# Optimization experiments

Hardware: AMD Instinct MI355X
Metric: run time of the kernel (lower is better)

Reference implementation:

```python
import jax, jax.numpy as jnp
import numpy as np

N_ATOMS = 10000
N_PAIRS = 100000
H = 64          # hidden_channels
R = 32          # number_of_radial_basis_functions
MAX_Z = 100
CUTOFF = 0.5    # nm (radial_max_distance), min = 0.0


def cosine_cutoff(d):
    # 0.5*(cos(pi*d/rc)+1) for d < rc else 0
    return jnp.where(d < CUTOFF, 0.5 * (jnp.cos(jnp.pi * d / CUTOFF) + 1.0), 0.0)


def expnormal_rbf(d):
    # ExpNormal smearing (TorchMD/TensorNet style), cutoff_lower = 0
    start = float(np.exp(-CUTOFF))
    means = jnp.linspace(start, 1.0, R, dtype=d.dtype)            # [R]
    beta = (2.0 / R * (1.0 - start)) ** -2
    alpha = 5.0 / CUTOFF
    return jnp.exp(-beta * (jnp.exp(-alpha * d)[:, None] - means) ** 2)  # [P,R]


def vector_to_skewtensor(v):
    x, y, z = v[:, 0], v[:, 1], v[:, 2]
    o = jnp.zeros_like(x)
    return jnp.stack([o, -z, y, z, o, -x, -y, x, o], axis=-1).reshape(-1, 3, 3)


def vector_to_symtensor(v):
    t = v[:, :, None] * v[:, None, :]                              # [P,3,3]
    tr3 = (t[:, 0, 0] + t[:, 1, 1] + t[:, 2, 2]) / 3.0
    return t - tr3[:, None, None] * jnp.eye(3, dtype=v.dtype)


def setup_inputs() -> dict:
    key = jax.random.key(0)
    ks = jax.random.split(key, 20)
    atomic_numbers = jax.random.randint(ks[0], (N_ATOMS,), 0, MAX_Z)
    pair_indices = jax.random.randint(ks[1], (2, N_PAIRS), 0, N_ATOMS)
    r_ij = jax.random.normal(ks[2], (N_PAIRS, 3), dtype=jnp.float32) * 0.12  # ~0.2 nm norms
    d_ij = jnp.linalg.norm(r_ij, axis=-1, keepdims=True) + 1e-6
    s = 0.1
    p = {
        'emb':    jax.random.normal(ks[3], (MAX_Z, H)) * s,
        'emb2_w': jax.random.normal(ks[4], (H, 2 * H)) * s,
        'emb2_b': jnp.zeros((H,)),
        'dp1_w':  jax.random.normal(ks[5], (H, R)) * s,
        'dp1_b':  jnp.zeros((H,)),
        'dp2_w':  jax.random.normal(ks[6], (H, R)) * s,
        'dp2_b':  jnp.zeros((H,)),
        'dp3_w':  jax.random.normal(ks[7], (H, R)) * s,
        'dp3_b':  jnp.zeros((H,)),
        'lt0_w':  jax.random.normal(ks[8], (H, H)) * s,
        'lt1_w':  jax.random.normal(ks[9], (H, H)) * s,
        'lt2_w':  jax.random.normal(ks[10], (H, H)) * s,
        'ls1_w':  jax.random.normal(ks[11], (2 * H, H)) * s,
        'ls1_b':  jnp.zeros((2 * H,)),
        'ls2_w':  jax.random.normal(ks[12], (3 * H, 2 * H)) * s,
        'ls2_b':  jnp.zeros((3 * H,)),
        'ln_g':   jnp.ones((H,)),
        'ln_b':   jnp.zeros((H,)),
    }
    return dict(atomic_numbers=atomic_numbers, pair_indices=pair_indices,
                d_ij=d_ij, r_ij=r_ij, **p)


def reference(atomic_numbers, pair_indices, d_ij, r_ij,
              emb, emb2_w, emb2_b, dp1_w, dp1_b, dp2_w, dp2_b, dp3_w, dp3_b,
              lt0_w, lt1_w, lt2_w, ls1_w, ls1_b, ls2_w, ls2_b, ln_g, ln_b):
    n_atoms = atomic_numbers.shape[0]
    src = pair_indices[0]
    # atomic number message Zij: concat(emb[i], emb[j]) -> Linear
    zi = emb[atomic_numbers]                                      # [N,H]
    zij = jnp.concatenate([zi[src], zi[pair_indices[1]]], axis=-1)  # [P,2H]
    Zij = zij @ emb2_w.T + emb2_b                                 # [P,H]
    d = d_ij[:, 0]                                                # [P]
    unit = r_ij / d_ij                                            # [P,3]
    rc = cosine_cutoff(d)                                         # [P]
    rbf = expnormal_rbf(d) * rc[:, None]                          # [P,R]
    C = rc[:, None] * Zij                                         # [P,H]
    f1 = (rbf @ dp1_w.T + dp1_b) * C                              # [P,H]
    f2 = (rbf @ dp2_w.T + dp2_b) * C * 10.0                       # Angstrom scale
    f3 = (rbf @ dp3_w.T + dp3_b) * C * 100.0
    eye = jnp.eye(3, dtype=r_ij.dtype)
    skew = vector_to_skewtensor(unit)                             # [P,3,3]
    sym = vector_to_symtensor(unit)                               # [P,3,3]
    Iij = f1[:, :, None, None] * eye                              # [P,H,3,3]
    Aij = f2[:, :, None, None] * skew[:, None]
    Sij = f3[:, :, None, None] * sym[:, None]
    I = jax.ops.segment_sum(Iij, src, num_segments=n_atoms)       # [N,H,3,3]
    A = jax.ops.segment_sum(Aij, src, num_segments=n_atoms)
    S = jax.ops.segment_sum(Sij, src, num_segments=n_atoms)
    # tensor_norm -> LayerNorm -> scalar MLP
    tn = jnp.sum((I + A + S) ** 2, axis=(-2, -1))                 # [N,H]
    mu = tn.mean(-1, keepdims=True)
    var = tn.var(-1, keepdims=True)
    norm = (tn - mu) / jnp.sqrt(var + 1e-5) * ln_g + ln_b
    norm = jax.nn.silu(norm @ ls1_w.T + ls1_b)
    norm = jax.nn.silu(norm @ ls2_w.T + ls2_b)                    # [N,3H]
    norm = norm.reshape(-1, H, 3)
    I = jnp.einsum('nhij,gh->ngij', I, lt0_w) * norm[:, :, 0][:, :, None, None]
    A = jnp.einsum('nhij,gh->ngij', A, lt1_w) * norm[:, :, 1][:, :, None, None]
    S = jnp.einsum('nhij,gh->ngij', S, lt2_w) * norm[:, :, 2][:, :, None, None]
    return I + A + S
```

## Files before the change

### kernel.cpp

```cpp
#include <hip/hip_runtime.h>
#include <hip/hip_bf16.h>

#define N_ATOMS 10000
#define N_PAIRS 100000
#define HH 64
#define MAXZ 100

typedef _Float16 h2_t __attribute__((ext_vector_type(2)));

constexpr float RBF_START = 0.6065306597126334f;
constexpr float RBF_STEP  = (1.0f - RBF_START) / 31.0f;
constexpr float RBF_BETA  = 1.0f / ((0.0625f * (1.0f - RBF_START)) * (0.0625f * (1.0f - RBF_START)));
constexpr float LOG2E     = 1.4426950408889634f;
constexpr float NEG_ALPHA_L2 = -10.0f * LOG2E;
constexpr float NEG_BETA_L2  = -RBF_BETA * LOG2E;

#define OFF_EMB   0
#define OFF_W2    6400
#define OFF_B2    14592
#define OFF_D1W   14656
#define OFF_D1B   16704
#define OFF_D2W   16768
#define OFF_D2B   18816
#define OFF_D3W   18880
#define OFF_D3B   20928
#define OFF_LT0   20992
#define OFF_LT1   25088
#define OFF_LT2   29184
#define OFF_L1W   33280
#define OFF_L1B   41472
#define OFF_L2W   41600
#define OFF_L2B   66176
#define OFF_LNG   66368
#define OFF_LNB   66432
#define N_PARAMF  66496

#define PH_DP   0
#define PH_L1   3072
#define PH_L2   7168
#define PH_LT   19456
#define PH_N    25600

#define WS_WF     0
#define WS_CNT    266240
#define WS_OFF    307200
#define WS_CUR    348160
#define WS_T1     389120
#define WS_T2     414720
#define WS_PH     440320
#define WS_DPK    542720
#define WS_ZNL    2142720
#define WS_RBF    2542720
#define WS_ACCH   8942720

__device__ __forceinline__ float bf2f(unsigned short u) {
    return __uint_as_float(((unsigned int)u) << 16);
}
__device__ __forceinline__ float fexp2(float x) { return __builtin_amdgcn_exp2f(x); }
__device__ __forceinline__ float fcos2pi(float x) { return __builtin_amdgcn_cosf(x); }
__device__ __forceinline__ float fsilu(float x) { return x / (1.0f + fexp2(-LOG2E * x)); }
__device__ __forceinline__ h2_t u2h(unsigned u) { return __builtin_bit_cast(h2_t, u); }
__device__ __forceinline__ unsigned packh2(float a, float b) {
    h2_t v; v.x = (_Float16)a; v.y = (_Float16)b;
    return __builtin_bit_cast(unsigned, v);
}

#if __has_builtin(__builtin_amdgcn_fdot2)
__device__ __forceinline__ float FDOT2(h2_t a, h2_t b, float c) {
    return __builtin_amdgcn_fdot2(a, b, c, false);
}
#else
__device__ __forceinline__ float FDOT2(h2_t a, h2_t b, float c) {
    return c + (float)a.x * (float)b.x + (float)a.y * (float)b.y;
}
#endif
__device__ __forceinline__ float dot16v(uint4 a, uint4 b, float acc) {
    acc = FDOT2(u2h(a.x), u2h(b.x), acc);
    acc = FDOT2(u2h(a.y), u2h(b.y), acc);
    acc = FDOT2(u2h(a.z), u2h(b.z), acc);
    acc = FDOT2(u2h(a.w), u2h(b.w), acc);
    return acc;
}
__device__ __forceinline__ float dot16h(const uint4* w, const uint4* x, float acc) {
    return dot16v(*w, *x, acc);
}

__device__ int classify64(const unsigned short* b, int lane) {
    unsigned short x = b[lane];
    int e = (x >> 7) & 0xFF;
    bool implaus = (x != 0) && (e < 96 || e > 133);
    bool zeroeven = ((lane & 1) == 0) && (x == 0);
    unsigned long long mi = __ballot(implaus);
    unsigned long long mz = __ballot(zeroeven);
    if (__popcll(mz) == 32) return 0;
    if (__popcll(mi) >= 8) return 0;
    return 1;
}

struct ConvArgs { const void* src[18]; float* dst; };

__global__ void k_prep(ConvArgs a, const int* __restrict__ pidx, int* __restrict__ cnt) {
    const int sizes[18] = {6400,8192,64,2048,64,2048,64,2048,64,4096,4096,4096,8192,128,24576,192,64,64};
    __shared__ int fl;
    if (threadIdx.x < 64) {
        int f = classify64((const unsigned short*)a.src[0], threadIdx.x);
        if (threadIdx.x == 0) fl = f;
    }
    __syncthreads();
    int t = blockIdx.x * 256 + threadIdx.x;
    if (t < N_PARAMF) {
        int acc = 0, seg = 0, off = t;
        #pragma unroll
        for (int i = 0; i < 18; ++i) {
            if (t >= acc && t < acc + sizes[i]) { seg = i; off = t - acc; }
            acc += sizes[i];
        }
        if (fl == 1) a.dst[t] = bf2f(((const unsigned short*)a.src[seg])[off]);
        else         a.dst[t] = ((const float*)a.src[seg])[off];
    }
    if (t < N_PAIRS) atomicAdd(&cnt[pidx[t]], 1);
}

__global__ void k_scantab(const float* __restrict__ WF, float* __restrict__ T1,
                          float* __restrict__ T2, unsigned* __restrict__ PH,
                          const int* __restrict__ cnt, int* __restrict__ offs,
                          int* __restrict__ cur) {
    __shared__ int buf[1024];
    if (blockIdx.x == 0) {
        int tid = threadIdx.x;
        int base = tid * 10;
        int c[10]; int s = 0;
        #pragma unroll
        for (int i = 0; i < 10; ++i) {
            int idx = base + i;
            int v = (idx < N_ATOMS) ? cnt[idx] : 0;
            c[i] = v; s += v;
        }
        buf[tid] = s;
        __syncthreads();
        for (int off = 1; off < 1024; off <<= 1) {
            int v = (tid >= off) ? buf[tid - off] : 0;
            __syncthreads();
            buf[tid] += v;
            __syncthreads();
        }
        int run = buf[tid] - s;
        #pragma unroll
        for (int i = 0; i < 10; ++i) {
            int idx = base + i;
            if (idx < N_ATOMS) { offs[idx] = run; cur[idx] = run; run += c[i]; }
        }
        if (tid == 0) offs[N_ATOMS] = N_PAIRS;
        return;
    }
    int t = (blockIdx.x - 1) * 1024 + threadIdx.x;
    if (t < 6400) {
        int z = t >> 6, h = t & 63;
        const float* ez = WF + OFF_EMB + z * HH;
        const float* w2 = WF + OFF_W2 + h * 128;
        float s1 = 0.f, s2 = 0.f;
        #pragma unroll
        for (int k = 0; k < 64; ++k) {
            float e = ez[k];
            s1 += w2[k] * e;
            s2 += w2[64 + k] * e;
        }
        T1[z * HH + h] = s1;
        T2[z * HH + h] = s2;
    }
    if (t < PH_N) {
        int src;
        if (t < PH_L1) {
            int w = t >> 10, r = t & 1023;
            src = (w == 0 ? OFF_D1W : (w == 1 ? OFF_D2W : OFF_D3W)) + r * 2;
        } else if (t < PH_L2) {
            src = OFF_L1W + (t - PH_L1) * 2;
        } else if (t < PH_LT) {
            src = OFF_L2W + (t - PH_L2) * 2;
        } else {
            src = OFF_LT0 + (t - PH_LT) * 2;
        }
        PH[t] = packh2(WF[src], WF[src + 1]);
    }
}

__global__ void k_fill(const int* __restrict__ pidx, const int* __restrict__ an,
                       const void* __restrict__ dij_v, const void* __restrict__ rij_v,
                       int* __restrict__ cur,
                       float4* __restrict__ dpack, int* __restrict__ znl,
                       unsigned* __restrict__ rbfp) {
    __shared__ int fdr[2];
    if (threadIdx.x < 64) {
        int fd = classify64((const unsigned short*)dij_v, threadIdx.x);
        int fr = classify64((const unsigned short*)rij_v, threadIdx.x);
        if (threadIdx.x == 0) { fdr[0] = fd; fdr[1] = fr; }
    }
    __syncthreads();
    int p = blockIdx.x * 256 + threadIdx.x;
    if (p >= N_PAIRS) return;
    int s = pidx[p];
    int dst = pidx[N_PAIRS + p];
    int pos = atomicAdd(&cur[s], 1);
    float d, rx, ry, rz;
    if (fdr[0] == 1) d = bf2f(((const unsigned short*)dij_v)[p]);
    else             d = ((const float*)dij_v)[p];
    if (fdr[1] == 1) {
        const unsigned short* r = (const unsigned short*)rij_v;
        rx = bf2f(r[3*p]); ry = bf2f(r[3*p+1]); rz = bf2f(r[3*p+2]);
    } else {
        const float* r = (const float*)rij_v;
        rx = r[3*p]; ry = r[3*p+1]; rz = r[3*p+2];
    }
    float inv = 1.0f / d;
    float rc = (d < 0.5f) ? 0.5f * (fcos2pi(d) + 1.0f) : 0.0f;
    dpack[pos] = make_float4(rx * inv, ry * inv, rz * inv, rc);
    znl[pos] = an[dst];
    float en = fexp2(NEG_ALPHA_L2 * d);
    unsigned* rp = rbfp + pos * 16;
    #pragma unroll
    for (int r2 = 0; r2 < 16; ++r2) {
        float t0 = en - (RBF_START + RBF_STEP * (float)(2 * r2));
        float t1 = en - (RBF_START + RBF_STEP * (float)(2 * r2 + 1));
        float v0 = fexp2(NEG_BETA_L2 * t0 * t0) * rc;
        float v1 = fexp2(NEG_BETA_L2 * t1 * t1) * rc;
        rp[r2] = packh2(v0, v1);
    }
}

__global__ __launch_bounds__(256, 2) void k_pair(
    const int* __restrict__ an,
    const float* __restrict__ WF,
    const int* __restrict__ offs,
    const float4* __restrict__ dpack, const int* __restrict__ znl,
    const unsigned* __restrict__ rbfp,
    const float* __restrict__ T1, const float* __restrict__ T2,
    const unsigned* __restrict__ PH,
    unsigned* __restrict__ accH)
{
    const int wave = threadIdx.x >> 6;
    const int h    = threadIdx.x & 63;
    const int n    = blockIdx.x * 4 + wave;

    const uint4* wp = (const uint4*)(PH + PH_DP);
    const uint4 w10 = wp[        h * 4 + 0], w11 = wp[        h * 4 + 1],
                w12 = wp[        h * 4 + 2], w13 = wp[        h * 4 + 3];
    const uint4 w20 = wp[256 +   h * 4 + 0], w21 = wp[256 +   h * 4 + 1],
                w22 = wp[256 +   h * 4 + 2], w23 = wp[256 +   h * 4 + 3];
    const uint4 w30 = wp[512 +   h * 4 + 0], w31 = wp[512 +   h * 4 + 1],
                w32 = wp[512 +   h * 4 + 2], w33 = wp[512 +   h * 4 + 3];

    const float ed1 = (WF + OFF_D1B)[h];
    const float ed2 = (WF + OFF_D2B)[h];
    const float ed3 = (WF + OFF_D3B)[h];
    const float zA  = (WF + OFF_B2)[h] + T1[an[n] * HH + h];

    float Is=0.f, sx=0.f, sy=0.f, sz=0.f;
    float Sxx=0.f, Syy=0.f, Szz=0.f, Sxy=0.f, Sxz=0.f, Syz=0.f;

    const int pbeg = offs[n], pend = offs[n + 1];
    const uint4* rbase = (const uint4*)rbfp;

    float4 dp_cur = make_float4(0.f, 0.f, 0.f, 0.f);
    uint4  r0c = {0,0,0,0}, r1c = {0,0,0,0}, r2c = {0,0,0,0}, r3c = {0,0,0,0};
    float  t2cur = 0.f;
    int    zn_n  = 0;
    if (pbeg < pend) {
        dp_cur = dpack[pbeg];
        r0c = rbase[pbeg*4+0]; r1c = rbase[pbeg*4+1];
        r2c = rbase[pbeg*4+2]; r3c = rbase[pbeg*4+3];
        t2cur = T2[znl[pbeg] * HH + h];
        if (pbeg + 1 < pend) zn_n = znl[pbeg + 1];
    }

    for (int ii = pbeg; ii < pend; ++ii) {
        const float4 dpv = dp_cur;
        const uint4  b0 = r0c, b1 = r1c, b2 = r2c, b3 = r3c;
        const float  t2v = t2cur;
        if (ii + 1 < pend) {
            dp_cur = dpack[ii + 1];
            r0c = rbase[(ii+1)*4+0]; r1c = rbase[(ii+1)*4+1];
            r2c = rbase[(ii+1)*4+2]; r3c = rbase[(ii+1)*4+3];
            t2cur = T2[zn_n * HH + h];
            if (ii + 2 < pend) zn_n = znl[ii + 2];
        }

        float g1 = ed1, g2 = ed2, g3 = ed3;
        g1 = dot16v(w10, b0, g1); g1 = dot16v(w11, b1, g1);
        g1 = dot16v(w12, b2, g1); g1 = dot16v(w13, b3, g1);
        g2 = dot16v(w20, b0, g2); g2 = dot16v(w21, b1, g2);
        g2 = dot16v(w22, b2, g2); g2 = dot16v(w23, b3, g2);
        g3 = dot16v(w30, b0, g3); g3 = dot16v(w31, b1, g3);
        g3 = dot16v(w32, b2, g3); g3 = dot16v(w33, b3, g3);

        float ux = dpv.x, uy = dpv.y, uz = dpv.z, rc = dpv.w;
        float Cc = rc * (zA + t2v);
        float f1 = g1 * Cc;
        float f2 = g2 * Cc * 10.0f;
        float f3 = g3 * Cc * 100.0f;

        Is += f1;
        sx += f2 * ux;  sy += f2 * uy;  sz += f2 * uz;
        float q = (ux*ux + uy*uy + uz*uz) * (1.0f / 3.0f);
        Sxx += f3 * (ux*ux - q);
        Syy += f3 * (uy*uy - q);
        Szz += f3 * (uz*uz - q);
        Sxy += f3 * (ux*uy);
        Sxz += f3 * (ux*uz);
        Syz += f3 * (uy*uz);
    }

    float tn = 3.0f*Is*Is + 2.0f*(sx*sx + sy*sy + sz*sz)
             + Sxx*Sxx + Syy*Syy + Szz*Szz
             + 2.0f*(Sxy*Sxy + Sxz*Sxz + Syz*Syz);
    float s1 = tn, s2 = tn * tn;
    #pragma unroll
    for (int o = 32; o > 0; o >>= 1) {
        s1 += __shfl_xor(s1, o);
        s2 += __shfl_xor(s2, o);
    }
    float mu  = s1 * (1.0f / 64.0f);
    float var = s2 * (1.0f / 64.0f) - mu * mu;
    float nv  = (tn - mu) * rsqrtf(var + 1e-5f) * (WF + OFF_LNG)[h] + (WF + OFF_LNB)[h];

    float vals[11] = {Is, sx, sy, sz, Sxx, Syy, Szz, Sxy, Sxz, Syz, nv};
    #pragma unroll
    for (int c = 0; c < 11; ++c) {
        float pv = __shfl_xor(vals[c], 1);
        if ((h & 1) == 0)
            accH[((n * 11 + c) << 5) + (h >> 1)] = packh2(vals[c], pv);
    }
}

__global__ __launch_bounds__(256, 2) void k_post(
    const float* __restrict__ WF,
    const unsigned* __restrict__ PH,
    const unsigned* __restrict__ accH,
    float* __restrict__ out)
{
    __shared__ __align__(16) unsigned wL2[192 * 68];
    __shared__ __align__(16) unsigned acch[4][12 * 32];
    __shared__ __align__(16) unsigned y1h[4][64];
    __shared__ __align__(16) unsigned y2h[4][96];

    for (int q = threadIdx.x; q < 12288; q += 256) {
        int m = q >> 6, u = q & 63;
        wL2[m * 68 + u] = PH[PH_L2 + q];
    }
    __syncthreads();

    const int wave = threadIdx.x >> 6;
    const int h    = threadIdx.x & 63;
    const int gw   = blockIdx.x * 4 + wave;
    const int GW   = gridDim.x * 4;

    const uint4* l1base = (const uint4*)(PH + PH_L1);
    const uint4* lt0 = (const uint4*)(PH + PH_LT) + h * 8;
    const uint4* lt1 = (const uint4*)(PH + PH_LT + 2048) + h * 8;
    const uint4* lt2 = (const uint4*)(PH + PH_LT + 4096) + h * 8;

    for (int n = gw; n < N_ATOMS; n += GW) {
        if (h < 32) {
            #pragma unroll
            for (int c = 0; c < 11; ++c)
                acch[wave][c * 32 + h] = accH[((n * 11 + c) << 5) + h];
        }
        __builtin_amdgcn_wave_barrier();

        const uint4* nvh = (const uint4*)&acch[wave][10 * 32];

        float ya = (WF + OFF_L1B)[h];
        float yb = (WF + OFF_L1B)[h + 64];
        {
            const uint4* ra = l1base + h * 8;
            const uint4* rb = l1base + (h + 64) * 8;
            #pragma unroll
            for (int k = 0; k < 8; ++k) {
                ya = dot16h(ra + k, nvh + k, ya);
                yb = dot16h(rb + k, nvh + k, yb);
            }
        }
        ya = fsilu(ya); yb = fsilu(yb);
        {
            float pa = __shfl_xor(ya, 1);
            float pb = __shfl_xor(yb, 1);
            if ((h & 1) == 0) {
                y1h[wave][(h >> 1)]      = packh2(ya, pa);
                y1h[wave][32 + (h >> 1)] = packh2(yb, pb);
            }
        }
        __builtin_amdgcn_wave_barrier();

        const uint4* y1p = (const uint4*)&y1h[wave][0];
        float z0 = (WF + OFF_L2B)[h];
        float z1 = (WF + OFF_L2B)[h + 64];
        float z2 = (WF + OFF_L2B)[h + 128];
        {
            const uint4* r0 = (const uint4*)&wL2[(h)       * 68];
            const uint4* r1 = (const uint4*)&wL2[(h + 64)  * 68];
            const uint4* r2 = (const uint4*)&wL2[(h + 128) * 68];
            #pragma unroll
            for (int k = 0; k < 16; ++k) {
                uint4 x = y1p[k];
                z0 = dot16v(r0[k], x, z0);
                z1 = dot16v(r1[k], x, z1);
                z2 = dot16v(r2[k], x, z2);
            }
        }
        z0 = fsilu(z0); z1 = fsilu(z1); z2 = fsilu(z2);
        {
            float p0 = __shfl_xor(z0, 1);
            float p1 = __shfl_xor(z1, 1);
            float p2 = __shfl_xor(z2, 1);
            if ((h & 1) == 0) {
                y2h[wave][(h >> 1)]      = packh2(z0, p0);
                y2h[wave][32 + (h >> 1)] = packh2(z1, p1);
                y2h[wave][64 + (h >> 1)] = packh2(z2, p2);
            }
        }
        __builtin_amdgcn_wave_barrier();

        float n0, n1, n2;
        {
            int i0 = 3 * h;
            unsigned u0 = y2h[wave][i0 >> 1];
            unsigned u1 = y2h[wave][(i0 >> 1) + 1];
            h2_t a = u2h(u0), b = u2h(u1);
            if (i0 & 1) { n0 = (float)a.y; n1 = (float)b.x; n2 = (float)b.y; }
            else        { n0 = (float)a.x; n1 = (float)a.y; n2 = (float)b.x; }
        }

        const uint4* aI  = (const uint4*)&acch[wave][0];
        const uint4* aAx = (const uint4*)&acch[wave][32];
        const uint4* aAy = (const uint4*)&acch[wave][64];
        const uint4* aAz = (const uint4*)&acch[wave][96];
        const uint4* aXX = (const uint4*)&acch[wave][128];
        const uint4* aYY = (const uint4*)&acch[wave][160];
        const uint4* aZZ = (const uint4*)&acch[wave][192];
        const uint4* aXY = (const uint4*)&acch[wave][224];
        const uint4* aXZ = (const uint4*)&acch[wave][256];
        const uint4* aYZ = (const uint4*)&acch[wave][288];

        float P0=0.f, PAx=0.f, PAy=0.f, PAz=0.f;
        float Q0=0.f, Q1=0.f, Q2=0.f, Q3=0.f, Q4=0.f, Q5=0.f;
        #pragma unroll
        for (int k = 0; k < 8; ++k) {
            P0  = dot16h(lt0 + k, aI  + k, P0);
            PAx = dot16h(lt1 + k, aAx + k, PAx);
            PAy = dot16h(lt1 + k, aAy + k, PAy);
            PAz = dot16h(lt1 + k, aAz + k, PAz);
            Q0  = dot16h(lt2 + k, aXX + k, Q0);
            Q1  = dot16h(lt2 + k, aYY + k, Q1);
            Q2  = dot16h(lt2 + k, aZZ + k, Q2);
            Q3  = dot16h(lt2 + k, aXY + k, Q3);
            Q4  = dot16h(lt2 + k, aXZ + k, Q4);
            Q5  = dot16h(lt2 + k, aYZ + k, Q5);
        }
        float Iv = P0 * n0;
        float Ax = PAx * n1, Ay = PAy * n1, Az = PAz * n1;
        float Xx = Q0 * n2, Yy = Q1 * n2, Zz = Q2 * n2;
        float Xy = Q3 * n2, Xz = Q4 * n2, Yz = Q5 * n2;

        float* o = out + (size_t)n * 576 + h * 9;
        o[0] =  Iv + Xx;  o[1] = -Az + Xy;  o[2] =  Ay + Xz;
        o[3] =  Az + Xy;  o[4] =  Iv + Yy;  o[5] = -Ax + Yz;
        o[6] = -Ay + Xz;  o[7] =  Ax + Yz;  o[8] =  Iv + Zz;
        __builtin_amdgcn_wave_barrier();
    }
}

extern "C" void kernel_launch(void* const* d_in, const int* in_sizes, int n_in,
                              void* d_out, int out_size, void* d_ws, size_t ws_size,
                              hipStream_t stream) {
    const int* an   = (const int*)d_in[0];
    const int* pidx = (const int*)d_in[1];

    char* ws = (char*)d_ws;
    float*    WF    = (float*)(ws + WS_WF);
    int*      cnt   = (int*)(ws + WS_CNT);
    int*      offs  = (int*)(ws + WS_OFF);
    int*      cur   = (int*)(ws + WS_CUR);
    float*    T1    = (float*)(ws + WS_T1);
    float*    T2    = (float*)(ws + WS_T2);
    unsigned* PH    = (unsigned*)(ws + WS_PH);
    float4*   dpack = (float4*)(ws + WS_DPK);
    int*      znl   = (int*)(ws + WS_ZNL);
    unsigned* rbfp  = (unsigned*)(ws + WS_RBF);
    unsigned* accH  = (unsigned*)(ws + WS_ACCH);
    float*    out   = (float*)d_out;

    hipMemsetAsync(cnt, 0, N_ATOMS * sizeof(int), stream);

    ConvArgs ca;
    for (int i = 0; i < 18; ++i) ca.src[i] = d_in[4 + i];
    ca.dst = WF;
    k_prep<<<(N_PAIRS + 255) / 256, 256, 0, stream>>>(ca, pidx, cnt);
    k_scantab<<<26, 1024, 0, stream>>>(WF, T1, T2, PH, cnt, offs, cur);
    k_fill<<<(N_PAIRS + 255) / 256, 256, 0, stream>>>(pidx, an, d_in[2], d_in[3],
                                                      cur, dpack, znl, rbfp);
    k_pair<<<2500, 256, 0, stream>>>(an, WF, offs, dpack, znl, rbfp, T1, T2, PH, accH);
    k_post<<<512, 256, 0, stream>>>(WF, PH, accH, out);
}
```

Baseline: 210.4 us.

## Compute RBF and cutoff in pair kernel via LDS instead of materialising buffer

```diff
diff --git a/kernel.cpp b/kernel.cpp
--- a/kernel.cpp
+++ b/kernel.cpp
@@ -50,8 +50,7 @@
 #define WS_PH     440320
 #define WS_DPK    542720
 #define WS_ZNL    2142720
-#define WS_RBF    2542720
-#define WS_ACCH   8942720
+#define WS_ACCH   2542720
 
 __device__ __forceinline__ float bf2f(unsigned short u) {
     return __uint_as_float(((unsigned int)u) << 16);
@@ -187,8 +186,7 @@
 __global__ void k_fill(const int* __restrict__ pidx, const int* __restrict__ an,
                        const void* __restrict__ dij_v, const void* __restrict__ rij_v,
                        int* __restrict__ cur,
-                       float4* __restrict__ dpack, int* __restrict__ znl,
-                       unsigned* __restrict__ rbfp) {
+                       float4* __restrict__ dpack, int* __restrict__ znl) {
     __shared__ int fdr[2];
     if (threadIdx.x < 64) {
         int fd = classify64((const unsigned short*)dij_v, threadIdx.x);
@@ -212,19 +210,8 @@
         rx = r[3*p]; ry = r[3*p+1]; rz = r[3*p+2];
     }
     float inv = 1.0f / d;
-    float rc = (d < 0.5f) ? 0.5f * (fcos2pi(d) + 1.0f) : 0.0f;
-    dpack[pos] = make_float4(rx * inv, ry * inv, rz * inv, rc);
+    dpack[pos] = make_float4(rx * inv, ry * inv, rz * inv, d);
     znl[pos] = an[dst];
-    float en = fexp2(NEG_ALPHA_L2 * d);
-    unsigned* rp = rbfp + pos * 16;
-    #pragma unroll
-    for (int r2 = 0; r2 < 16; ++r2) {
-        float t0 = en - (RBF_START + RBF_STEP * (float)(2 * r2));
-        float t1 = en - (RBF_START + RBF_STEP * (float)(2 * r2 + 1));
-        float v0 = fexp2(NEG_BETA_L2 * t0 * t0) * rc;
-        float v1 = fexp2(NEG_BETA_L2 * t1 * t1) * rc;
-        rp[r2] = packh2(v0, v1);
-    }
 }
 
 __global__ __launch_bounds__(256, 2) void k_pair(
@@ -232,14 +219,14 @@
     const float* __restrict__ WF,
     const int* __restrict__ offs,
     const float4* __restrict__ dpack, const int* __restrict__ znl,
-    const unsigned* __restrict__ rbfp,
     const float* __restrict__ T1, const float* __restrict__ T2,
     const unsigned* __restrict__ PH,
     unsigned* __restrict__ accH)
 {
+    __shared__ __align__(16) unsigned rbuf[4][2][16];
+
     const int wave = threadIdx.x >> 6;
     const int h    = threadIdx.x & 63;
-    const int n    = blockIdx.x * 4 + wave;
 
     const uint4* wp = (const uint4*)(PH + PH_DP);
     const uint4 w10 = wp[        h * 4 + 0], w11 = wp[        h * 4 + 1],
@@ -252,82 +239,109 @@
     const float ed1 = (WF + OFF_D1B)[h];
     const float ed2 = (WF + OFF_D2B)[h];
     const float ed3 = (WF + OFF_D3B)[h];
-    const float zA  = (WF + OFF_B2)[h] + T1[an[n] * HH + h];
-
-    float Is=0.f, sx=0.f, sy=0.f, sz=0.f;
-    float Sxx=0.f, Syy=0.f, Szz=0.f, Sxy=0.f, Sxz=0.f, Syz=0.f;
-
-    const int pbeg = offs[n], pend = offs[n + 1];
-    const uint4* rbase = (const uint4*)rbfp;
-
-    float4 dp_cur = make_float4(0.f, 0.f, 0.f, 0.f);
-    uint4  r0c = {0,0,0,0}, r1c = {0,0,0,0}, r2c = {0,0,0,0}, r3c = {0,0,0,0};
-    float  t2cur = 0.f;
-    int    zn_n  = 0;
-    if (pbeg < pend) {
-        dp_cur = dpack[pbeg];
-        r0c = rbase[pbeg*4+0]; r1c = rbase[pbeg*4+1];
-        r2c = rbase[pbeg*4+2]; r3c = rbase[pbeg*4+3];
-        t2cur = T2[znl[pbeg] * HH + h];
-        if (pbeg + 1 < pend) zn_n = znl[pbeg + 1];
-    }
-
-    for (int ii = pbeg; ii < pend; ++ii) {
-        const float4 dpv = dp_cur;
-        const uint4  b0 = r0c, b1 = r1c, b2 = r2c, b3 = r3c;
-        const float  t2v = t2cur;
-        if (ii + 1 < pend) {
-            dp_cur = dpack[ii + 1];
-            r0c = rbase[(ii+1)*4+0]; r1c = rbase[(ii+1)*4+1];
-            r2c = rbase[(ii+1)*4+2]; r3c = rbase[(ii+1)*4+3];
-            t2cur = T2[zn_n * HH + h];
-            if (ii + 2 < pend) zn_n = znl[ii + 2];
-        }
-
-        float g1 = ed1, g2 = ed2, g3 = ed3;
-        g1 = dot16v(w10, b0, g1); g1 = dot16v(w11, b1, g1);
-        g1 = dot16v(w12, b2, g1); g1 = dot16v(w13, b3, g1);
-        g2 = dot16v(w20, b0, g2); g2 = dot16v(w21, b1, g2);
-        g2 = dot16v(w22, b2, g2); g2 = dot16v(w23, b3, g2);
-        g3 = dot16v(w30, b0, g3); g3 = dot16v(w31, b1, g3);
-        g3 = dot16v(w32, b2, g3); g3 = dot16v(w33, b3, g3);
-
-        float ux = dpv.x, uy = dpv.y, uz = dpv.z, rc = dpv.w;
-        float Cc = rc * (zA + t2v);
-        float f1 = g1 * Cc;
-        float f2 = g2 * Cc * 10.0f;
-        float f3 = g3 * Cc * 100.0f;
-
-        Is += f1;
-        sx += f2 * ux;  sy += f2 * uy;  sz += f2 * uz;
-        float q = (ux*ux + uy*uy + uz*uz) * (1.0f / 3.0f);
-        Sxx += f3 * (ux*ux - q);
-        Syy += f3 * (uy*uy - q);
-        Szz += f3 * (uz*uz - q);
-        Sxy += f3 * (ux*uy);
-        Sxz += f3 * (ux*uz);
-        Syz += f3 * (uy*uz);
-    }
-
-    float tn = 3.0f*Is*Is + 2.0f*(sx*sx + sy*sy + sz*sz)
-             + Sxx*Sxx + Syy*Syy + Szz*Szz
-             + 2.0f*(Sxy*Sxy + Sxz*Sxz + Syz*Syz);
-    float s1 = tn, s2 = tn * tn;
-    #pragma unroll
-    for (int o = 32; o > 0; o >>= 1) {
-        s1 += __shfl_xor(s1, o);
-        s2 += __shfl_xor(s2, o);
-    }
-    float mu  = s1 * (1.0f / 64.0f);
-    float var = s2 * (1.0f / 64.0f) - mu * mu;
-    float nv  = (tn - mu) * rsqrtf(var + 1e-5f) * (WF + OFF_LNG)[h] + (WF + OFF_LNB)[h];
-
-    float vals[11] = {Is, sx, sy, sz, Sxx, Syy, Szz, Sxy, Sxz, Syz, nv};
-    #pragma unroll
-    for (int c = 0; c < 11; ++c) {
-        float pv = __shfl_xor(vals[c], 1);
-        if ((h & 1) == 0)
-            accH[((n * 11 + c) << 5) + (h >> 1)] = packh2(vals[c], pv);
+    const float eb2 = (WF + OFF_B2)[h];
+    const float lng = (WF + OFF_LNG)[h];
+    const float lnb = (WF + OFF_LNB)[h];
+
+    unsigned* sl0 = &rbuf[wave][0][0];
+    unsigned* sl1 = &rbuf[wave][1][0];
+    const int stride = gridDim.x * 4;
+
+    for (int n = blockIdx.x * 4 + wave; n < N_ATOMS; n += stride) {
+        const float zA = eb2 + T1[an[n] * HH + h];
+        const int pbeg = offs[n];
+        const int len  = offs[n + 1] - pbeg;
+
+        float Is=0.f, sx=0.f, sy=0.f, sz=0.f;
+        float Sxx=0.f, Syy=0.f, Szz=0.f, Sxy=0.f, Sxz=0.f, Syz=0.f;
+
+        float4 dc = make_float4(0,0,0,0), dn = make_float4(0,0,0,0);
+        float tc = 0.f, t2n = 0.f, rc_c = 0.f, rc_n = 0.f;
+        if (len > 0) { dc = dpack[pbeg];     tc  = T2[znl[pbeg] * HH + h]; }
+        if (len > 1) { dn = dpack[pbeg + 1]; t2n = T2[znl[pbeg + 1] * HH + h]; }
+        if (len > 0) {
+            float d = dc.w;
+            rc_c = (d < 0.5f) ? 0.5f * (fcos2pi(d) + 1.0f) : 0.0f;
+            float en = fexp2(NEG_ALPHA_L2 * d);
+            if (h < 16) {
+                float t0 = en - (RBF_START + RBF_STEP * (float)(2 * h));
+                float t1 = en - (RBF_START + RBF_STEP * (float)(2 * h + 1));
+                sl0[h] = packh2(fexp2(NEG_BETA_L2 * t0 * t0) * rc_c,
+                                fexp2(NEG_BETA_L2 * t1 * t1) * rc_c);
+            }
+        }
+        __builtin_amdgcn_wave_barrier();
+
+        for (int ii = 0; ii < len; ++ii) {
+            if (ii + 1 < len) {
+                float d = dn.w;
+                rc_n = (d < 0.5f) ? 0.5f * (fcos2pi(d) + 1.0f) : 0.0f;
+                float en = fexp2(NEG_ALPHA_L2 * d);
+                unsigned* sl = (ii & 1) ? sl0 : sl1;
+                if (h < 16) {
+                    float t0 = en - (RBF_START + RBF_STEP * (float)(2 * h));
+                    float t1 = en - (RBF_START + RBF_STEP * (float)(2 * h + 1));
+                    sl[h] = packh2(fexp2(NEG_BETA_L2 * t0 * t0) * rc_n,
+                                   fexp2(NEG_BETA_L2 * t1 * t1) * rc_n);
+                }
+            }
+            float4 d2v = make_float4(0,0,0,0); float t2v2 = 0.f;
+            bool has2 = (ii + 2 < len);
+            if (has2) {
+                d2v  = dpack[pbeg + ii + 2];
+                t2v2 = T2[znl[pbeg + ii + 2] * HH + h];
+            }
+            const uint4* rbp = (const uint4*)((ii & 1) ? sl1 : sl0);
+            uint4 b0 = rbp[0], b1 = rbp[1], b2 = rbp[2], b3 = rbp[3];
+            float g1 = ed1, g2 = ed2, g3 = ed3;
+            g1 = dot16v(w10, b0, g1); g1 = dot16v(w11, b1, g1);
+            g1 = dot16v(w12, b2, g1); g1 = dot16v(w13, b3, g1);
+            g2 = dot16v(w20, b0, g2); g2 = dot16v(w21, b1, g2);
+            g2 = dot16v(w22, b2, g2); g2 = dot16v(w23, b3, g2);
+            g3 = dot16v(w30, b0, g3); g3 = dot16v(w31, b1, g3);
+            g3 = dot16v(w32, b2, g3); g3 = dot16v(w33, b3, g3);
+
+            float ux = dc.x, uy = dc.y, uz = dc.z;
+            float Cc = rc_c * (zA + tc);
+            float f1 = g1 * Cc;
+            float f2 = g2 * Cc * 10.0f;
+            float f3 = g3 * Cc * 100.0f;
+
+            Is += f1;
+            sx += f2 * ux;  sy += f2 * uy;  sz += f2 * uz;
+            float q = (ux*ux + uy*uy + uz*uz) * (1.0f / 3.0f);
+            Sxx += f3 * (ux*ux - q);
+            Syy += f3 * (uy*uy - q);
+            Szz += f3 * (uz*uz - q);
+            Sxy += f3 * (ux*uy);
+            Sxz += f3 * (ux*uz);
+            Syz += f3 * (uy*uz);
+
+            dc = dn; tc = t2n; rc_c = rc_n;
+            if (has2) { dn = d2v; t2n = t2v2; }
+            __builtin_amdgcn_wave_barrier();
+        }
+
+        float tn = 3.0f*Is*Is + 2.0f*(sx*sx + sy*sy + sz*sz)
+                 + Sxx*Sxx + Syy*Syy + Szz*Szz
+                 + 2.0f*(Sxy*Sxy + Sxz*Sxz + Syz*Syz);
+        float s1 = tn, s2 = tn * tn;
+        #pragma unroll
+        for (int o = 32; o > 0; o >>= 1) {
+            s1 += __shfl_xor(s1, o);
+            s2 += __shfl_xor(s2, o);
+        }
+        float mu  = s1 * (1.0f / 64.0f);
+        float var = s2 * (1.0f / 64.0f) - mu * mu;
+        float nv  = (tn - mu) * rsqrtf(var + 1e-5f) * lng + lnb;
+
+        float vals[11] = {Is, sx, sy, sz, Sxx, Syy, Szz, Sxy, Sxz, Syz, nv};
+        #pragma unroll
+        for (int c = 0; c < 11; ++c) {
+            float pv = __shfl_xor(vals[c], 1);
+            if ((h & 1) == 0)
+                accH[((n * 11 + c) << 5) + (h >> 1)] = packh2(vals[c], pv);
+        }
     }
 }
 
@@ -484,7 +498,6 @@
     unsigned* PH    = (unsigned*)(ws + WS_PH);
     float4*   dpack = (float4*)(ws + WS_DPK);
     int*      znl   = (int*)(ws + WS_ZNL);
-    unsigned* rbfp  = (unsigned*)(ws + WS_RBF);
     unsigned* accH  = (unsigned*)(ws + WS_ACCH);
     float*    out   = (float*)d_out;
 
@@ -496,7 +509,7 @@
     k_prep<<<(N_PAIRS + 255) / 256, 256, 0, stream>>>(ca, pidx, cnt);
     k_scantab<<<26, 1024, 0, stream>>>(WF, T1, T2, PH, cnt, offs, cur);
     k_fill<<<(N_PAIRS + 255) / 256, 256, 0, stream>>>(pidx, an, d_in[2], d_in[3],
-                                                      cur, dpack, znl, rbfp);
-    k_pair<<<2500, 256, 0, stream>>>(an, WF, offs, dpack, znl, rbfp, T1, T2, PH, accH);
+                                                      cur, dpack, znl);
+    k_pair<<<768, 256, 0, stream>>>(an, WF, offs, dpack, znl, T1, T2, PH, accH);
     k_post<<<512, 256, 0, stream>>>(WF, PH, accH, out);
 }
```

New measurement: 213.4 us. About the same (+1.4%).
